# Performance work log

Measured on AMD Instinct MI355X. Metric: run time of the kernel, lower is better.

The kernel has to match this reference:

```python
import jax, jax.numpy as jnp
import numpy as np

ALPHA = 50.0
EPS = 1e-12  # torch F.normalize eps


def setup_inputs() -> dict:
    key = jax.random.key(0)
    k1, k2 = jax.random.split(key)
    N, C, H, W_sp, K = 64, 128, 64, 64, 64
    x = jax.random.normal(k1, (N, C, H, W_sp), dtype=jnp.float32)
    # centroids.permute(1,0): shape [C, K]; orthogonal-ish init approximated by scaled gaussian
    W = jax.random.normal(k2, (C, K), dtype=jnp.float32) * (1.0 / np.sqrt(C))
    bias = jnp.zeros((K,), dtype=jnp.float32)
    return {"x": x, "W": W, "bias": bias}


def _l2norm(v, axis):
    return v / jnp.maximum(jnp.linalg.norm(v, axis=axis, keepdims=True), EPS)


def reference(x, W, bias):
    N, C, H, W_sp = x.shape
    K = W.shape[1]
    x = _l2norm(x, axis=1)                      # normalize over channels
    xf = x.reshape(N, C, H * W_sp)              # [N, C, P]
    Wn = _l2norm(W, axis=0)                     # column-normalized weight [C, K]
    # soft assignment logits, computed directly in [N, K, P] layout
    sa_logits = jnp.einsum('ncp,ck->nkp', xf, Wn)
    sa = jax.nn.softmax((sa_logits + bias[None, :, None]) * ALPHA, axis=1)  # over clusters
    # VLAD via two GEMM-like contractions instead of the [N,K,C,P] residual tensor:
    # vlad[n,k,c] = sum_p sa[n,k,p] * xf[n,c,p] - W[c,k] * sum_p sa[n,k,p]
    vlad = jnp.einsum('nkp,ncp->nkc', sa, xf) - sa.sum(axis=-1)[:, :, None] * W.T[None]
    vlad = _l2norm(vlad, axis=2)                # intra-normalize per cluster
    vlad = vlad.reshape(N, K * C)
    vlad = _l2norm(vlad, axis=1)                # global L2
    return (vlad, sa_logits)                    # original returns soft_assign_ permuted to [N, K, P]
```

## Files before the change

### kernel.cpp

```cpp
#include <hip/hip_runtime.h>
#include <math.h>

#define ALPHA 50.0f
#define EPS 1e-12f

constexpr int N = 64, C = 128, P = 4096, K = 64;
constexpr int NCH2 = 8;

typedef short short8_t __attribute__((ext_vector_type(8)));
typedef short short4_t __attribute__((ext_vector_type(4)));
typedef float f4 __attribute__((ext_vector_type(4)));
typedef unsigned int u32x4 __attribute__((ext_vector_type(4)));
typedef unsigned int u32x2 __attribute__((ext_vector_type(2)));

__device__ __forceinline__ unsigned short f2bf(float f) {
    union { float f; unsigned u; } v; v.f = f;
    unsigned r = (v.u + 0x7FFFu + ((v.u >> 16) & 1u)) >> 16;
    return (unsigned short)r;
}

__device__ __forceinline__ unsigned cvtpk(float lo, float hi) {
    unsigned r;
    asm("v_cvt_pk_bf16_f32 %0, %1, %2" : "=v"(r) : "v"(lo), "v"(hi));
    return r;
}

__device__ __forceinline__ void bar_lds() {
    asm volatile("s_waitcnt lgkmcnt(0)" ::: "memory");
    __builtin_amdgcn_s_barrier();
}

__global__ __launch_bounds__(256) void k_prep(
    const float* __restrict__ W, unsigned short* __restrict__ wnT,
    float* __restrict__ ss2acc)
{
    __shared__ float Wl[C * 65];
    __shared__ float red[256];
    __shared__ float cinv[K];
    const int tid = threadIdx.x;
    if (tid < K) ss2acc[tid] = 0.f;
    for (int idx = tid; idx < C * K; idx += 256) {
        int c = idx >> 6, k = idx & 63;
        Wl[c * 65 + k] = W[idx];
    }
    __syncthreads();
    {
        const int k = tid & 63, part = tid >> 6;
        float s = 0.f;
        #pragma unroll
        for (int i = 0; i < 32; ++i) {
            float v = Wl[(part * 32 + i) * 65 + k];
            s = fmaf(v, v, s);
        }
        red[tid] = s;
    }
    __syncthreads();
    if (tid < K)
        cinv[tid] = 1.0f / fmaxf(
            sqrtf(red[tid] + red[64 + tid] + red[128 + tid] + red[192 + tid]), EPS);
    __syncthreads();
    for (int idx = tid; idx < K * C; idx += 256) {
        int k = idx >> 7, c = idx & 127;
        wnT[idx] = f2bf(Wl[c * 65 + k] * cinv[k]);
    }
}

__global__ __launch_bounds__(256, 2) void k_fused(
    const float* __restrict__ x, const unsigned short* __restrict__ wnT,
    const float* __restrict__ bias, float* __restrict__ logits,
    float* __restrict__ vlad_part, float* __restrict__ Spart)
{
    __shared__ unsigned short xsT[64 * 136];
    __shared__ unsigned short xsN[128 * 76];
    __shared__ float          saf[64 * 66];
    __shared__ unsigned short sa2s[64 * 72];
    __shared__ float denom[16][65];
    __shared__ float invs[64];
    __shared__ float rfin[64];
    __shared__ float red[256];
    __shared__ float biass[64];

    const int tid  = threadIdx.x;
    const int n    = blockIdx.x >> 3;
    const int blk8 = blockIdx.x & 7;
    const int pbase = blk8 * 512;

    const int w = tid >> 6, lane = tid & 63;
    const int q = lane >> 4, l15 = lane & 15;
    const int pxg = tid & 15, cg = tid >> 4;
    const int px = tid & 63, sq = tid >> 6;

    if (tid < K) biass[tid] = bias[tid] * ALPHA;

    short8_t af[4];
    #pragma unroll
    for (int c0 = 0; c0 < 4; ++c0)
        af[c0] = *(const short8_t*)&wnT[(16 * w + l15) * 128 + c0 * 32 + 8 * q];

    f4 acc2[8];
    #pragma unroll
    for (int ct = 0; ct < 8; ++ct) acc2[ct] = (f4){0.f, 0.f, 0.f, 0.f};
    float Sreg = 0.f;

    const float* xrow = x + (size_t)n * C * P + pbase + 4 * pxg;

    float4 va[8], vb[8];
    #pragma unroll
    for (int j = 0; j < 8; ++j) va[j] = *(const float4*)&xrow[(size_t)(8 * cg + j) * P];

    for (int ch = 0; ch < 8; ++ch) {
        if (ch < 7) {
            const float* xb = xrow + (ch + 1) * 64;
            #pragma unroll
            for (int j = 0; j < 8; ++j)
                vb[j] = *(const float4*)&xb[(size_t)(8 * cg + j) * P];
        }
        bar_lds();
        const int p0 = pbase + ch * 64;
        const float* vf = (const float*)va;

        float pss[4] = {0.f, 0.f, 0.f, 0.f};
        #pragma unroll
        for (int j = 0; j < 8; ++j)
            #pragma unroll
            for (int i = 0; i < 4; ++i)
                pss[i] = fmaf(vf[j * 4 + i], vf[j * 4 + i], pss[i]);
        float* red2 = saf;
        #pragma unroll
        for (int i = 0; i < 4; ++i) red2[(4 * pxg + i) * 16 + cg] = pss[i];

        #pragma unroll
        for (int i = 0; i < 4; ++i) {
            u32x4 t;
            #pragma unroll
            for (int jj = 0; jj < 4; ++jj)
                t[jj] = cvtpk(vf[(2 * jj) * 4 + i], vf[(2 * jj + 1) * 4 + i]);
            *(u32x4*)&xsT[(4 * pxg + i) * 136 + 8 * cg] = t;
        }
        #pragma unroll
        for (int j = 0; j < 8; ++j) {
            u32x2 t;
            t[0] = cvtpk(vf[j * 4 + 0], vf[j * 4 + 1]);
            t[1] = cvtpk(vf[j * 4 + 2], vf[j * 4 + 3]);
            *(u32x2*)&xsN[(8 * cg + j) * 76 + 4 * pxg] = t;
        }
        bar_lds();
        if (tid < 64) {
            float s = 0.f;
            #pragma unroll
            for (int g = 0; g < 16; ++g) s += red2[tid * 16 + g];
            invs[tid] = 1.0f / fmaxf(sqrtf(s), EPS);
        }
        bar_lds();

        f4 acc1[4];
        #pragma unroll
        for (int t = 0; t < 4; ++t) acc1[t] = (f4){0.f, 0.f, 0.f, 0.f};
        #pragma unroll
        for (int c0 = 0; c0 < 4; ++c0)
            #pragma unroll
            for (int pxt = 0; pxt < 4; ++pxt) {
                short8_t bf = *(const short8_t*)&xsT[(pxt * 16 + l15) * 136 + c0 * 32 + 8 * q];
                acc1[pxt] = __builtin_amdgcn_mfma_f32_16x16x32_bf16(af[c0], bf, acc1[pxt], 0, 0, 0);
            }

        float* lgp = logits + (size_t)n * K * P + p0;
        float bz[4];
        #pragma unroll
        for (int r = 0; r < 4; ++r) bz[r] = biass[16 * w + 4 * q + r];
        #pragma unroll
        for (int pxt = 0; pxt < 4; ++pxt) {
            const int pxl = pxt * 16 + l15;
            const float iv = invs[pxl];
            float psum = 0.f;
            #pragma unroll
            for (int r = 0; r < 4; ++r) {
                const int k = 16 * w + 4 * q + r;
                const float lv = acc1[pxt][r] * iv;
                lgp[(size_t)k * P + pxl] = lv;
                const float e = __expf(fmaf(lv, ALPHA, bz[r]));
                saf[k * 66 + pxl] = e;
                psum += e;
            }
            denom[4 * w + q][pxl] = psum;
        }
        bar_lds();
        if (tid < 64) {
            float d = 0.f;
            #pragma unroll
            for (int g = 0; g < 16; ++g) d += denom[g][tid];
            rfin[tid] = 1.0f / d;
        }
        bar_lds();

        {
            float s = 0.f;
            #pragma unroll
            for (int ii = 0; ii < 16; ++ii)
                s += saf[px * 66 + sq * 16 + ii] * rfin[sq * 16 + ii];
            Sreg += s;
        }
        {
            const float rf = rfin[px] * invs[px];
            #pragma unroll
            for (int kk = 0; kk < 16; ++kk) {
                const int k = sq * 16 + kk;
                sa2s[k * 72 + px] = f2bf(saf[k * 66 + px] * rf);
            }
        }
        bar_lds();

        short8_t a2[2];
        #pragma unroll
        for (int kit = 0; kit < 2; ++kit)
            a2[kit] = *(const short8_t*)&sa2s[(16 * w + l15) * 72 + kit * 32 + 8 * q];
        #pragma unroll
        for (int ct = 0; ct < 8; ++ct)
            #pragma unroll
            for (int kit = 0; kit < 2; ++kit) {
                const unsigned short* bp = &xsN[(ct * 16 + l15) * 76 + kit * 32 + 8 * q];
                short4_t b0 = *(const short4_t*)bp;
                short4_t b1 = *(const short4_t*)(bp + 4);
                short8_t bb;
                bb[0] = b0[0]; bb[1] = b0[1]; bb[2] = b0[2]; bb[3] = b0[3];
                bb[4] = b1[0]; bb[5] = b1[1]; bb[6] = b1[2]; bb[7] = b1[3];
                acc2[ct] = __builtin_amdgcn_mfma_f32_16x16x32_bf16(a2[kit], bb, acc2[ct], 0, 0, 0);
            }

        if (ch < 7) {
            #pragma unroll
            for (int j = 0; j < 8; ++j) va[j] = vb[j];
        }
    }

    float* vp = vlad_part + ((size_t)blk8 * N + n) * (size_t)(K * C);
    #pragma unroll
    for (int ct = 0; ct < 8; ++ct)
        #pragma unroll
        for (int r = 0; r < 4; ++r)
            vp[(16 * w + 4 * q + r) * C + ct * 16 + l15] = acc2[ct][r];

    red[tid] = Sreg;
    __syncthreads();
    if (tid < 64)
        Spart[((size_t)blk8 * N + n) * K + tid] =
            red[tid] + red[64 + tid] + red[128 + tid] + red[192 + tid];
}

__global__ __launch_bounds__(256) void k_post1(
    const float* __restrict__ vlad_part, const float* __restrict__ W,
    const float* __restrict__ Spart, float* __restrict__ out,
    float* __restrict__ ss2acc)
{
    __shared__ float red[16];
    const int tid = threadIdx.x;
    const int n  = blockIdx.x >> 2;
    const int kq = blockIdx.x & 3;
    const int kl = tid >> 4;
    const int ci = tid & 15;
    const int k  = kq * 16 + kl;
    const int c0 = ci * 8;

    float Sk = 0.f;
    #pragma unroll
    for (int ch = 0; ch < NCH2; ++ch) Sk += Spart[(size_t)(ch * N + n) * K + k];

    float v[8];
    #pragma unroll
    for (int l = 0; l < 8; ++l) v[l] = 0.f;
    #pragma unroll
    for (int ch = 0; ch < NCH2; ++ch) {
        const float* vp = vlad_part + ((size_t)(ch * N + n) * K + k) * C + c0;
        float4 a = *(const float4*)&vp[0];
        float4 b = *(const float4*)&vp[4];
        v[0] += a.x; v[1] += a.y; v[2] += a.z; v[3] += a.w;
        v[4] += b.x; v[5] += b.y; v[6] += b.z; v[7] += b.w;
    }

    float ss = 0.f;
    #pragma unroll
    for (int l = 0; l < 8; ++l) {
        float val = v[l] - W[(size_t)(c0 + l) * K + k] * Sk;
        v[l] = val;
        ss = fmaf(val, val, ss);
    }
    ss += __shfl_xor(ss, 1);
    ss += __shfl_xor(ss, 2);
    ss += __shfl_xor(ss, 4);
    ss += __shfl_xor(ss, 8);
    const float inv1 = 1.0f / fmaxf(sqrtf(ss), EPS);
    float ss2 = 0.f;
    #pragma unroll
    for (int l = 0; l < 8; ++l) { v[l] *= inv1; ss2 = fmaf(v[l], v[l], ss2); }
    ss2 += __shfl_xor(ss2, 1);
    ss2 += __shfl_xor(ss2, 2);
    ss2 += __shfl_xor(ss2, 4);
    ss2 += __shfl_xor(ss2, 8);
    if (ci == 0) red[kl] = ss2;
    __syncthreads();
    if (tid == 0) {
        float t = 0.f;
        #pragma unroll
        for (int i = 0; i < 16; ++i) t += red[i];
        atomicAdd(&ss2acc[n], t);
    }

    float* op = out + (size_t)n * K * C + (size_t)k * C + c0;
    *(float4*)&op[0] = (float4){v[0], v[1], v[2], v[3]};
    *(float4*)&op[4] = (float4){v[4], v[5], v[6], v[7]};
}

__global__ __launch_bounds__(256) void k_post2(
    float* __restrict__ out, const float* __restrict__ ss2acc)
{
    const int n   = blockIdx.x >> 2;
    const int seg = blockIdx.x & 3;
    const float inv2 = 1.0f / fmaxf(sqrtf(ss2acc[n]), EPS);
    float* p = out + (size_t)n * K * C + (size_t)seg * 2048 + (size_t)threadIdx.x * 8;
    float4 a = *(const float4*)&p[0];
    float4 b = *(const float4*)&p[4];
    a.x *= inv2; a.y *= inv2; a.z *= inv2; a.w *= inv2;
    b.x *= inv2; b.y *= inv2; b.z *= inv2; b.w *= inv2;
    *(float4*)&p[0] = a;
    *(float4*)&p[4] = b;
}

extern "C" void kernel_launch(void* const* d_in, const int* in_sizes, int n_in,
                              void* d_out, int out_size, void* d_ws, size_t ws_size,
                              hipStream_t stream)
{
    const float* x    = (const float*)d_in[0];
    const float* W    = (const float*)d_in[1];
    const float* bias = (const float*)d_in[2];

    float* out_vlad   = (float*)d_out;
    float* out_logits = (float*)d_out + (size_t)N * K * C;

    unsigned short* wnT = (unsigned short*)d_ws;
    float* ss2acc       = (float*)((char*)d_ws + 16384);
    float* Spart        = (float*)((char*)d_ws + 32768);
    float* vlad_part    = (float*)((char*)d_ws + 32768 + 131072);

    k_prep<<<dim3(1), dim3(256), 0, stream>>>(W, wnT, ss2acc);
    k_fused<<<dim3(N * NCH2), dim3(256), 0, stream>>>(x, wnT, bias, out_logits, vlad_part, Spart);
    k_post1<<<dim3(N * 4), dim3(256), 0, stream>>>(vlad_part, W, Spart, out_vlad, ss2acc);
    k_post2<<<dim3(N * 4), dim3(256), 0, stream>>>(out_vlad, ss2acc);
}
```

Before: 241.9 us.

## Fold weight normalization into fused kernel and swizzle LDS layouts

```diff
diff --git a/kernel.cpp b/kernel.cpp
--- a/kernel.cpp
+++ b/kernel.cpp
@@ -30,55 +30,24 @@
     __builtin_amdgcn_s_barrier();
 }
 
-__global__ __launch_bounds__(256) void k_prep(
-    const float* __restrict__ W, unsigned short* __restrict__ wnT,
+__global__ __launch_bounds__(256, 2) void k_fused(
+    const float* __restrict__ x, const float* __restrict__ W,
+    const float* __restrict__ bias, float* __restrict__ logits,
+    float* __restrict__ vlad_part, float* __restrict__ Spart,
     float* __restrict__ ss2acc)
 {
-    __shared__ float Wl[C * 65];
-    __shared__ float red[256];
-    __shared__ float cinv[K];
-    const int tid = threadIdx.x;
-    if (tid < K) ss2acc[tid] = 0.f;
-    for (int idx = tid; idx < C * K; idx += 256) {
-        int c = idx >> 6, k = idx & 63;
-        Wl[c * 65 + k] = W[idx];
-    }
-    __syncthreads();
-    {
-        const int k = tid & 63, part = tid >> 6;
-        float s = 0.f;
-        #pragma unroll
-        for (int i = 0; i < 32; ++i) {
-            float v = Wl[(part * 32 + i) * 65 + k];
-            s = fmaf(v, v, s);
-        }
-        red[tid] = s;
-    }
-    __syncthreads();
-    if (tid < K)
-        cinv[tid] = 1.0f / fmaxf(
-            sqrtf(red[tid] + red[64 + tid] + red[128 + tid] + red[192 + tid]), EPS);
-    __syncthreads();
-    for (int idx = tid; idx < K * C; idx += 256) {
-        int k = idx >> 7, c = idx & 127;
-        wnT[idx] = f2bf(Wl[c * 65 + k] * cinv[k]);
-    }
-}
-
-__global__ __launch_bounds__(256, 2) void k_fused(
-    const float* __restrict__ x, const unsigned short* __restrict__ wnT,
-    const float* __restrict__ bias, float* __restrict__ logits,
-    float* __restrict__ vlad_part, float* __restrict__ Spart)
-{
-    __shared__ unsigned short xsT[64 * 136];
-    __shared__ unsigned short xsN[128 * 76];
-    __shared__ float          saf[64 * 66];
-    __shared__ unsigned short sa2s[64 * 72];
-    __shared__ float denom[16][65];
-    __shared__ float invs[64];
-    __shared__ float rfin[64];
-    __shared__ float red[256];
-    __shared__ float biass[64];
+    __shared__ __align__(16) char smem[69632];
+    unsigned short* xsT  = (unsigned short*)smem;
+    unsigned short* xsN  = (unsigned short*)(smem + 17408);
+    float*          saf  = (float*)(smem + 36864);
+    unsigned short* sa2s = (unsigned short*)(smem + 54272);
+    float*          denom= (float*)(smem + 63488);
+    float*          invs = (float*)(smem + 67840);
+    float*          rfin = (float*)(smem + 68096);
+    float*          red  = (float*)(smem + 68352);
+    float*          biass= (float*)(smem + 69376);
+    float*          Wl   = (float*)smem;
+    unsigned short* wnl  = (unsigned short*)(smem + 36864);
 
     const int tid  = threadIdx.x;
     const int n    = blockIdx.x >> 3;
@@ -88,25 +57,62 @@
     const int w = tid >> 6, lane = tid & 63;
     const int q = lane >> 4, l15 = lane & 15;
     const int pxg = tid & 15, cg = tid >> 4;
-    const int px = tid & 63, sq = tid >> 6;
-
+
+    if (blockIdx.x == 0 && tid < 64) ss2acc[tid] = 0.f;
     if (tid < K) biass[tid] = bias[tid] * ALPHA;
 
+    const float* xrow = x + (size_t)n * C * P + pbase + 4 * pxg;
+    float4 va[8], vb[8];
     short8_t af[4];
-    #pragma unroll
-    for (int c0 = 0; c0 < 4; ++c0)
-        af[c0] = *(const short8_t*)&wnT[(16 * w + l15) * 128 + c0 * 32 + 8 * q];
+
+    {
+        float4 wv[8];
+        #pragma unroll
+        for (int it = 0; it < 8; ++it)
+            wv[it] = *(const float4*)&W[(size_t)(tid + it * 256) * 4];
+        #pragma unroll
+        for (int j = 0; j < 8; ++j)
+            va[j] = *(const float4*)&xrow[(size_t)(8 * cg + j) * P];
+        #pragma unroll
+        for (int it = 0; it < 8; ++it) {
+            const int idx4 = tid + it * 256;
+            *(float4*)&Wl[(idx4 >> 4) * 68 + (idx4 & 15) * 4] = wv[it];
+        }
+        bar_lds();
+        {
+            const int k = tid & 63, part = tid >> 6;
+            float s = 0.f;
+            #pragma unroll
+            for (int i = 0; i < 32; ++i) {
+                float v = Wl[(part * 32 + i) * 68 + k];
+                s = fmaf(v, v, s);
+            }
+            red[tid] = s;
+        }
+        bar_lds();
+        if (tid < 64)
+            invs[tid] = 1.0f / fmaxf(
+                sqrtf(red[tid] + red[64 + tid] + red[128 + tid] + red[192 + tid]), EPS);
+        bar_lds();
+        #pragma unroll
+        for (int it = 0; it < 32; ++it) {
+            const int idx = tid + it * 256;
+            const int k = idx >> 7, c = idx & 127;
+            wnl[k * 128 + c] = f2bf(Wl[c * 68 + k] * invs[k]);
+        }
+        bar_lds();
+        #pragma unroll
+        for (int c0 = 0; c0 < 4; ++c0)
+            af[c0] = *(const short8_t*)&wnl[(16 * w + l15) * 128 + c0 * 32 + 8 * q];
+    }
 
     f4 acc2[8];
     #pragma unroll
     for (int ct = 0; ct < 8; ++ct) acc2[ct] = (f4){0.f, 0.f, 0.f, 0.f};
     float Sreg = 0.f;
 
-    const float* xrow = x + (size_t)n * C * P + pbase + 4 * pxg;
-
-    float4 va[8], vb[8];
-    #pragma unroll
-    for (int j = 0; j < 8; ++j) va[j] = *(const float4*)&xrow[(size_t)(8 * cg + j) * P];
+    const int pbT8 = 8 * (cg ^ (pxg & 7));
+    const int l4 = l15 >> 2;
 
     for (int ch = 0; ch < 8; ++ch) {
         if (ch < 7) {
@@ -125,9 +131,9 @@
             #pragma unroll
             for (int i = 0; i < 4; ++i)
                 pss[i] = fmaf(vf[j * 4 + i], vf[j * 4 + i], pss[i]);
-        float* red2 = saf;
-        #pragma unroll
-        for (int i = 0; i < 4; ++i) red2[(4 * pxg + i) * 16 + cg] = pss[i];
+        float* rd2 = saf;
+        #pragma unroll
+        for (int i = 0; i < 4; ++i) rd2[(4 * pxg + i) * 17 + cg] = pss[i];
 
         #pragma unroll
         for (int i = 0; i < 4; ++i) {
@@ -135,34 +141,37 @@
             #pragma unroll
             for (int jj = 0; jj < 4; ++jj)
                 t[jj] = cvtpk(vf[(2 * jj) * 4 + i], vf[(2 * jj + 1) * 4 + i]);
-            *(u32x4*)&xsT[(4 * pxg + i) * 136 + 8 * cg] = t;
+            *(u32x4*)&xsT[(4 * pxg + i) * 136 + pbT8] = t;
         }
         #pragma unroll
         for (int j = 0; j < 8; ++j) {
-            u32x2 t;
-            t[0] = cvtpk(vf[j * 4 + 0], vf[j * 4 + 1]);
-            t[1] = cvtpk(vf[j * 4 + 2], vf[j * 4 + 3]);
-            *(u32x2*)&xsN[(8 * cg + j) * 76 + 4 * pxg] = t;
-        }
-        bar_lds();
+            u32x2 t2;
+            t2[0] = cvtpk(vf[j * 4 + 0], vf[j * 4 + 1]);
+            t2[1] = cvtpk(vf[j * 4 + 2], vf[j * 4 + 3]);
+            *(u32x2*)&xsN[(8 * cg + j) * 76 + 4 * pxg] = t2;
+        }
+        bar_lds();
+
         if (tid < 64) {
             float s = 0.f;
             #pragma unroll
-            for (int g = 0; g < 16; ++g) s += red2[tid * 16 + g];
+            for (int g = 0; g < 16; ++g) s += rd2[tid * 17 + g];
             invs[tid] = 1.0f / fmaxf(sqrtf(s), EPS);
         }
-        bar_lds();
-
         f4 acc1[4];
         #pragma unroll
         for (int t = 0; t < 4; ++t) acc1[t] = (f4){0.f, 0.f, 0.f, 0.f};
+        __builtin_amdgcn_s_setprio(1);
         #pragma unroll
         for (int c0 = 0; c0 < 4; ++c0)
             #pragma unroll
             for (int pxt = 0; pxt < 4; ++pxt) {
-                short8_t bf = *(const short8_t*)&xsT[(pxt * 16 + l15) * 136 + c0 * 32 + 8 * q];
+                const int pb = (4 * c0 + q) ^ (4 * (pxt & 1) + l4);
+                short8_t bf = *(const short8_t*)&xsT[(pxt * 16 + l15) * 136 + pb * 8];
                 acc1[pxt] = __builtin_amdgcn_mfma_f32_16x16x32_bf16(af[c0], bf, acc1[pxt], 0, 0, 0);
             }
+        __builtin_amdgcn_s_setprio(0);
+        bar_lds();
 
         float* lgp = logits + (size_t)n * K * P + p0;
         float bz[4];
@@ -177,36 +186,45 @@
             for (int r = 0; r < 4; ++r) {
                 const int k = 16 * w + 4 * q + r;
                 const float lv = acc1[pxt][r] * iv;
-                lgp[(size_t)k * P + pxl] = lv;
+                __builtin_nontemporal_store(lv, &lgp[(size_t)k * P + pxl]);
                 const float e = __expf(fmaf(lv, ALPHA, bz[r]));
-                saf[k * 66 + pxl] = e;
+                saf[k * 68 + pxl] = e;
                 psum += e;
             }
-            denom[4 * w + q][pxl] = psum;
+            denom[(4 * w + q) * 68 + pxl] = psum;
         }
         bar_lds();
         if (tid < 64) {
             float d = 0.f;
             #pragma unroll
-            for (int g = 0; g < 16; ++g) d += denom[g][tid];
+            for (int g = 0; g < 16; ++g) d += denom[g * 68 + tid];
             rfin[tid] = 1.0f / d;
         }
         bar_lds();
 
         {
+            const float* sp = &saf[lane * 68 + 16 * w];
+            const float* rp = &rfin[16 * w];
+            const float* ip = &invs[16 * w];
             float s = 0.f;
-            #pragma unroll
-            for (int ii = 0; ii < 16; ++ii)
-                s += saf[px * 66 + sq * 16 + ii] * rfin[sq * 16 + ii];
+            unsigned pk[8];
+            #pragma unroll
+            for (int m = 0; m < 4; ++m) {
+                f4 e  = *(const f4*)&sp[4 * m];
+                f4 rf = *(const f4*)&rp[4 * m];
+                f4 iv = *(const f4*)&ip[4 * m];
+                s += e[0] * rf[0]; s += e[1] * rf[1];
+                s += e[2] * rf[2]; s += e[3] * rf[3];
+                const float v0 = e[0] * (rf[0] * iv[0]);
+                const float v1 = e[1] * (rf[1] * iv[1]);
+                const float v2 = e[2] * (rf[2] * iv[2]);
+                const float v3 = e[3] * (rf[3] * iv[3]);
+                pk[2 * m]     = cvtpk(v0, v1);
+                pk[2 * m + 1] = cvtpk(v2, v3);
+            }
             Sreg += s;
-        }
-        {
-            const float rf = rfin[px] * invs[px];
-            #pragma unroll
-            for (int kk = 0; kk < 16; ++kk) {
-                const int k = sq * 16 + kk;
-                sa2s[k * 72 + px] = f2bf(saf[k * 66 + px] * rf);
-            }
+            *(u32x4*)&sa2s[lane * 72 + 16 * w]     = (u32x4){pk[0], pk[1], pk[2], pk[3]};
+            *(u32x4*)&sa2s[lane * 72 + 16 * w + 8] = (u32x4){pk[4], pk[5], pk[6], pk[7]};
         }
         bar_lds();
 
@@ -214,6 +232,7 @@
         #pragma unroll
         for (int kit = 0; kit < 2; ++kit)
             a2[kit] = *(const short8_t*)&sa2s[(16 * w + l15) * 72 + kit * 32 + 8 * q];
+        __builtin_amdgcn_s_setprio(1);
         #pragma unroll
         for (int ct = 0; ct < 8; ++ct)
             #pragma unroll
@@ -226,6 +245,7 @@
                 bb[4] = b1[0]; bb[5] = b1[1]; bb[6] = b1[2]; bb[7] = b1[3];
                 acc2[ct] = __builtin_amdgcn_mfma_f32_16x16x32_bf16(a2[kit], bb, acc2[ct], 0, 0, 0);
             }
+        __builtin_amdgcn_s_setprio(0);
 
         if (ch < 7) {
             #pragma unroll
@@ -336,13 +356,12 @@
     float* out_vlad   = (float*)d_out;
     float* out_logits = (float*)d_out + (size_t)N * K * C;
 
-    unsigned short* wnT = (unsigned short*)d_ws;
-    float* ss2acc       = (float*)((char*)d_ws + 16384);
-    float* Spart        = (float*)((char*)d_ws + 32768);
-    float* vlad_part    = (float*)((char*)d_ws + 32768 + 131072);
-
-    k_prep<<<dim3(1), dim3(256), 0, stream>>>(W, wnT, ss2acc);
-    k_fused<<<dim3(N * NCH2), dim3(256), 0, stream>>>(x, wnT, bias, out_logits, vlad_part, Spart);
+    float* ss2acc     = (float*)((char*)d_ws + 16384);
+    float* Spart      = (float*)((char*)d_ws + 32768);
+    float* vlad_part  = (float*)((char*)d_ws + 32768 + 131072);
+
+    k_fused<<<dim3(N * NCH2), dim3(256), 0, stream>>>(
+        x, W, bias, out_logits, vlad_part, Spart, ss2acc);
     k_post1<<<dim3(N * 4), dim3(256), 0, stream>>>(vlad_part, W, Spart, out_vlad, ss2acc);
     k_post2<<<dim3(N * 4), dim3(256), 0, stream>>>(out_vlad, ss2acc);
 }
```

Measured after the change: 237.6 us. Within noise of the previous version (-1.8%).
